# Kernel tuning notes

Hardware: AMD Instinct MI355X
Metric: run time of the kernel (lower is better)

Reference implementation:

```python
import jax, jax.numpy as jnp
import numpy as np

D_MODEL = 1024
N_HEADS = 16
HEAD_DIM = D_MODEL // N_HEADS
MAX_POS = 4096
ROPE_BASE = 10000.0
NEG_INF = -1e30


def _rope_cache(max_pos, head_dim, base):
    inv_freq = 1.0 / (base ** (np.arange(0, head_dim, 2, dtype=np.float32) / head_dim))
    t = np.arange(max_pos, dtype=np.float32)[:, None] * inv_freq[None, :]  # [P, D/2]
    cos = np.repeat(np.cos(t), 2, axis=-1)  # [P, D] (repeat_interleave)
    sin = np.repeat(np.sin(t), 2, axis=-1)
    return jnp.asarray(cos), jnp.asarray(sin)

COS_CACHE, SIN_CACHE = _rope_cache(MAX_POS, HEAD_DIM, ROPE_BASE)


def _rotate_half(x):
    # interleaved pairs: (x0,x1,x2,x3,...) -> (-x1,x0,-x3,x2,...)
    x1 = x[..., ::2]
    x2 = x[..., 1::2]
    return jnp.stack((-x2, x1), axis=-1).reshape(x.shape)


def setup_inputs() -> dict:
    key = jax.random.key(0)
    k0, k1, k2 = jax.random.split(key, 3)
    B, S = 4, 1024
    hidden_states = jax.random.normal(k0, (B, S, D_MODEL), dtype=jnp.float32)
    positions = jnp.arange(S, dtype=jnp.int64 if jax.config.jax_enable_x64 else jnp.int32)
    causal_mask = jnp.triu(jnp.ones((S, S), dtype=bool), k=1)  # True above diagonal -> masked
    # learned params (torch nn.Linear weight layout: [out, in], y = x @ W.T)
    Wqkv = jax.random.normal(k1, (3 * D_MODEL, D_MODEL), dtype=jnp.float32) * (D_MODEL ** -0.5)
    Wout = jax.random.normal(k2, (D_MODEL, D_MODEL), dtype=jnp.float32) * (D_MODEL ** -0.5)
    return {"hidden_states": hidden_states, "positions": positions,
            "causal_mask": causal_mask, "Wqkv": Wqkv, "Wout": Wout}


def reference(hidden_states, positions, causal_mask, Wqkv, Wout):
    B, S, D = hidden_states.shape
    qkv = hidden_states @ Wqkv.T                                   # [B,S,3D]
    qkv = qkv.reshape(B, S, 3, N_HEADS, HEAD_DIM)
    qkv = jnp.transpose(qkv, (2, 0, 3, 1, 4))                      # [3,B,H,S,Dh]
    q, k, v = qkv[0], qkv[1], qkv[2]
    # RoPE
    pos = jnp.clip(positions, 0, MAX_POS - 1)
    if pos.ndim == 1:
        pos = pos[None, :]
    cos = COS_CACHE[pos][:, None, :, :].astype(q.dtype)            # [B,1,S,Dh]
    sin = SIN_CACHE[pos][:, None, :, :].astype(q.dtype)
    q = q * cos + _rotate_half(q) * sin
    k = k * cos + _rotate_half(k) * sin
    # SDPA with causal bias (F.scaled_dot_product_attention default scaling)
    scale = HEAD_DIM ** -0.5
    scores = jnp.einsum('bhqd,bhkd->bhqk', q, k) * scale           # [B,H,S,S]
    scores = jnp.where(causal_mask[None, None, :, :], NEG_INF, scores)
    probs = jax.nn.softmax(scores, axis=-1)
    attn = jnp.einsum('bhqk,bhkd->bhqd', probs, v)                 # [B,H,S,Dh]
    attn = jnp.transpose(attn, (0, 2, 1, 3)).reshape(B, S, D)
    return attn @ Wout.T
```

## Files before the change

kernel.cpp:

```cpp
#include <hip/hip_runtime.h>

typedef __attribute__((ext_vector_type(8))) short short8;
typedef __attribute__((ext_vector_type(4))) float f32x4;

#define MFMA(a, b, c) __builtin_amdgcn_mfma_f32_16x16x32_bf16((a), (b), (c), 0, 0, 0)

#define S_LEN 1024
#define DM 1024
#define NHEADS 16
#define HD 64
#define NBH 64
#define MAXPOS 4096

__device__ __forceinline__ ushort f2bf(float f) {
    unsigned u = __builtin_bit_cast(unsigned, f);
    u += 0x7fffu + ((u >> 16) & 1u);
    return (ushort)(u >> 16);
}
__device__ __forceinline__ float bf2f(ushort h) {
    return __builtin_bit_cast(float, (unsigned)h << 16);
}

__device__ __forceinline__ void gload16(const ushort* g, ushort* l) {
    __builtin_amdgcn_global_load_lds(
        (const __attribute__((address_space(1))) unsigned int*)g,
        (__attribute__((address_space(3))) unsigned int*)l, 16, 0, 0);
}

__global__ __launch_bounds__(256) void k_cvt3(const float4* __restrict__ hs,
                                              const float4* __restrict__ wqkv,
                                              const float4* __restrict__ wout,
                                              ushort4* __restrict__ hsB,
                                              ushort4* __restrict__ wqkvB,
                                              ushort4* __restrict__ woutB,
                                              float* __restrict__ tab) {
    int id = blockIdx.x * 256 + threadIdx.x;
    if (id < 2097152) {
        const float4* src;
        ushort4* dst;
        int off;
        if (id < 1048576)      { src = hs;   dst = hsB;   off = id; }
        else if (id < 1835008) { src = wqkv; dst = wqkvB; off = id - 1048576; }
        else                   { src = wout; dst = woutB; off = id - 1835008; }
        float4 v = src[off];
        ushort4 o;
        o.x = f2bf(v.x); o.y = f2bf(v.y); o.z = f2bf(v.z); o.w = f2bf(v.w);
        dst[off] = o;
    } else {
        int t = id - 2097152;
        int p = t >> 5, i = t & 31;
        float inv = powf(10000.f, -(float)(2 * i) / 64.f);
        float th = (float)p * inv;
        float s, c;
        sincosf(th, &s, &c);
        tab[2 * t] = c;
        tab[2 * t + 1] = s;
    }
}

template <int MODE>
__global__ __launch_bounds__(512, 6) void k_gemm(
    const ushort* __restrict__ A, const ushort* __restrict__ BT,
    float* __restrict__ Cf,
    const int* __restrict__ pos, const float* __restrict__ tab,
    ushort* __restrict__ Qh, ushort* __restrict__ Kh, ushort* __restrict__ Vt,
    int M, int N, int K, int nbx) {
    __shared__ __align__(16) ushort SH[3 * 8192];
    const int tid = threadIdx.x;
    const int lane = tid & 63, wave = tid >> 6;
    const int wr = wave >> 2, wc = wave & 3;
    const int l15 = lane & 15, lhi = lane >> 4;
    const int nby = gridDim.x / nbx;
    const int xcd = blockIdx.x & 7, idx = blockIdx.x >> 3;
    const int Creg = nbx >> 1, Rreg = nby >> 2;
    const int by = (xcd >> 1) * Rreg + idx / Creg;
    const int bx = (xcd & 1) * Creg + idx % Creg;
    const int m0 = by << 7, n0 = bx << 7;

    const int srow = tid >> 2;
    const int scol = (((tid & 3) ^ (srow & 3) ^ ((srow >> 2) & 3)) << 3);
    const int fcol = ((lhi ^ ((l15 & 3) ^ ((l15 >> 2) & 3)))) << 3;

    f32x4 acc[4][2];
#pragma unroll
    for (int i = 0; i < 4; ++i)
#pragma unroll
        for (int j = 0; j < 2; ++j) acc[i][j] = 0;

#define STAGE(bs, kb)                                                           \
    do {                                                                        \
        ushort* bb = SH + (bs) * 8192;                                          \
        gload16(&A[(size_t)(m0 + srow) * K + (kb) + scol], bb + tid * 8);       \
        gload16(&BT[(size_t)(n0 + srow) * K + (kb) + scol],                     \
                bb + 4096 + tid * 8);                                           \
    } while (0)

    const int nk = K >> 5;
    STAGE(0, 0);
    STAGE(1, 32);
    int bi = 0;
    for (int t = 0; t < nk; ++t) {
        if (t + 1 < nk) {
            asm volatile("s_waitcnt vmcnt(2)" ::: "memory");
        } else {
            asm volatile("s_waitcnt vmcnt(0)" ::: "memory");
        }
        __builtin_amdgcn_s_barrier();
        __builtin_amdgcn_sched_barrier(0);
        if (t + 2 < nk) {
            int bs = bi + 2;
            if (bs >= 3) bs -= 3;
            STAGE(bs, (t + 2) << 5);
        }
        const ushort* bufA = SH + bi * 8192;
        const ushort* bufB = bufA + 4096;
        short8 a[4], b[2];
#pragma unroll
        for (int fm = 0; fm < 4; ++fm)
            a[fm] = *(const short8*)&bufA[(wr * 64 + fm * 16 + l15) * 32 + fcol];
#pragma unroll
        for (int fn = 0; fn < 2; ++fn)
            b[fn] = *(const short8*)&bufB[(wc * 32 + fn * 16 + l15) * 32 + fcol];
#pragma unroll
        for (int fm = 0; fm < 4; ++fm)
#pragma unroll
            for (int fn = 0; fn < 2; ++fn)
                acc[fm][fn] = MFMA(a[fm], b[fn], acc[fm][fn]);
        bi = (bi == 2) ? 0 : bi + 1;
    }
#undef STAGE
    __syncthreads();

    if (MODE == 0) {
#pragma unroll
        for (int fm = 0; fm < 4; ++fm)
#pragma unroll
            for (int fn = 0; fn < 2; ++fn)
#pragma unroll
                for (int i = 0; i < 4; ++i) {
                    int row = m0 + wr * 64 + fm * 16 + lhi * 4 + i;
                    int col = n0 + wc * 32 + fn * 16 + l15;
                    Cf[(size_t)row * N + col] = acc[fm][fn][i];
                }
    } else {
        const int sec = n0 >> 10;
        if (sec < 2) {
            ushort* dstb = sec == 0 ? Qh : Kh;
            const float qs = sec == 0 ? 0.125f : 1.0f;
#pragma unroll
            for (int fm = 0; fm < 4; ++fm)
#pragma unroll
                for (int i = 0; i < 4; ++i) {
                    const int row = m0 + wr * 64 + fm * 16 + lhi * 4 + i;
                    const int b = row >> 10, s = row & 1023;
                    int p = pos[s];
                    p = p < 0 ? 0 : (p > MAXPOS - 1 ? MAXPOS - 1 : p);
#pragma unroll
                    for (int fn = 0; fn < 2; ++fn) {
                        const int col = n0 + wc * 32 + fn * 16 + l15;
                        const int cw = col & 1023;
                        const int h = cw >> 6, d = cw & 63;
                        const float c  = tab[((size_t)p * 32 + (d >> 1)) * 2];
                        const float sn = tab[((size_t)p * 32 + (d >> 1)) * 2 + 1];
                        const float v = acc[fm][fn][i];
                        const float pr = __shfl_xor(v, 1);
                        const float o = (d & 1) ? (v * c + pr * sn) : (v * c - pr * sn);
                        dstb[((size_t)((b * 16 + h) * 1024 + s)) * 64 + d] = f2bf(o * qs);
                    }
                }
        } else {
            ushort (*T)[132] = (ushort(*)[132]) & SH[0];
#pragma unroll
            for (int fm = 0; fm < 4; ++fm)
#pragma unroll
                for (int fn = 0; fn < 2; ++fn)
#pragma unroll
                    for (int i = 0; i < 4; ++i)
                        T[wr * 64 + fm * 16 + lhi * 4 + i][wc * 32 + fn * 16 + l15] =
                            f2bf(acc[fm][fn][i]);
            __syncthreads();
            const int b = m0 >> 10, s0 = m0 & 1023;
            const int dd = tid & 127, grp = tid >> 7;
            const int hv = ((n0 & 1023) >> 6) + (dd >> 6);
            const int d = dd & 63;
            ushort* dst = Vt + ((size_t)(b * 16 + hv) * 64 + d) * S_LEN + s0;
#pragma unroll
            for (int j = 0; j < 4; ++j) {
                const int ch = grp * 4 + j;
                __align__(16) ushort tmp[8];
#pragma unroll
                for (int e = 0; e < 8; ++e) tmp[e] = T[ch * 8 + e][dd];
                *(uint4*)&dst[ch * 8] = *(uint4*)tmp;
            }
        }
    }
}

__global__ __launch_bounds__(256, 2) void k_attn(const ushort* __restrict__ Qh,
                                                 const ushort* __restrict__ Kh,
                                                 const ushort* __restrict__ Vt,
                                                 ushort* __restrict__ attnB) {
    __shared__ __align__(16) ushort Ks[2][128][64];
    __shared__ __align__(16) ushort Vs[2][64][128];
    __shared__ __align__(16) ushort P[4][16][128];
    const int bh = blockIdx.x;
    const int g  = blockIdx.y;
    const int gA = g, gB = 15 - g;
    const int nkbA = (gA + 2) >> 1;
    const int nkbB = (gB + 2) >> 1;
    const int tid = threadIdx.x;
    const int wave = tid >> 6, lane = tid & 63;
    const int l15 = lane & 15, lhi = lane >> 4;
    const int b = bh >> 4, h = bh & 15;
    const ushort* Qp = Qh + (size_t)bh * S_LEN * 64;
    const ushort* Kp = Kh + (size_t)bh * S_LEN * 64;
    const ushort* Vp = Vt + (size_t)bh * 64 * S_LEN;
    const int qbA = (gA << 6) + (wave << 4);
    const int qbB = (gB << 6) + (wave << 4);
    const int qrowbA = qbA + lhi * 4;
    const int qrowbB = qbB + lhi * 4;

    ushort* KsF = &Ks[0][0][0];
    ushort* VsF = &Vs[0][0][0];
    ushort* Pw  = &P[wave][0][0];

    short8 aQA0 = *(const short8*)&Qp[(size_t)(qbA + l15) * 64 + lhi * 8];
    short8 aQA1 = *(const short8*)&Qp[(size_t)(qbA + l15) * 64 + 32 + lhi * 8];
    short8 aQB0 = *(const short8*)&Qp[(size_t)(qbB + l15) * 64 + lhi * 8];
    short8 aQB1 = *(const short8*)&Qp[(size_t)(qbB + l15) * 64 + 32 + lhi * 8];

    short8 ones;
#pragma unroll
    for (int j = 0; j < 8; ++j) ones[j] = (short)0x3F80;

    f32x4 OA0{}, OA1{}, OA2{}, OA3{}, ssumA{};
    f32x4 OB0{}, OB1{}, OB2{}, OB3{}, ssumB{};

#define STAGEKV(bo, k0s)                                                        \
    do {                                                                        \
        _Pragma("unroll") for (int k = 0; k < 4; ++k) {                         \
            const int u = tid + k * 256;                                        \
            const int r = u >> 3, c = u & 7;                                    \
            gload16(&Kp[(size_t)((k0s) + r) * 64 + ((c ^ (r & 7)) << 3)],       \
                    KsF + (bo) + u * 8);                                        \
        }                                                                       \
        _Pragma("unroll") for (int k = 0; k < 4; ++k) {                         \
            const int u = tid + k * 256;                                        \
            const int r = u >> 4, c = u & 15;                                   \
            const int cs = c ^ (r & 7);                                         \
            gload16(&Vp[(size_t)r * S_LEN + (k0s) + cs * 8], VsF + (bo) + u * 8); \
        }                                                                       \
    } while (0)

#define LDSK(s, kk) (*(const short8*)(KsF + (cur << 13) + ((((s) << 4) + l15) << 6) + \
                                      (((((kk) << 2) + lhi) ^ (l15 & 7)) << 3)))
#define LDSV(n, kk) (*(const short8*)(VsF + (cur << 13) + ((((n) << 4) + l15) << 7) + \
                                      (((((kk) << 2) + lhi) ^ (l15 & 7)) << 3)))

    STAGEKV(0, 0);
    __syncthreads();

    int cur = 0;
    for (int kb = 0; kb < nkbB; ++kb) {
        const int k0 = kb << 7;
        if (kb + 1 < nkbB) STAGEKV((cur ^ 1) << 13, k0 + 128);

#define TILE_WORK(AQ0, AQ1, QROWB, NKB, O0, O1, O2, O3, SSUM)                   \
    if (kb < (NKB)) {                                                           \
        f32x4 sc[8];                                                            \
        __builtin_amdgcn_s_setprio(1);                                          \
        _Pragma("unroll") for (int s = 0; s < 8; ++s) {                         \
            sc[s] = f32x4{0.f, 0.f, 0.f, 0.f};                                  \
            sc[s] = MFMA(AQ0, LDSK(s, 0), sc[s]);                               \
            sc[s] = MFMA(AQ1, LDSK(s, 1), sc[s]);                               \
        }                                                                       \
        __builtin_amdgcn_s_setprio(0);                                          \
        if (kb == (NKB) - 1) {                                                  \
            _Pragma("unroll") for (int s = 0; s < 8; ++s)                       \
                _Pragma("unroll") for (int i = 0; i < 4; ++i) {                 \
                    float v = sc[s][i];                                         \
                    if (k0 + s * 16 + l15 > (QROWB) + i) v = -1e30f;            \
                    const int row = lhi * 4 + i;                                \
                    Pw[row * 128 +                                              \
                       (((s * 2 + (l15 >> 3)) ^ (row & 7)) << 3) + (l15 & 7)] = \
                        f2bf(__expf(v - 8.f));                                  \
                }                                                               \
        } else {                                                                \
            _Pragma("unroll") for (int s = 0; s < 8; ++s)                       \
                _Pragma("unroll") for (int i = 0; i < 4; ++i) {                 \
                    const int row = lhi * 4 + i;                                \
                    Pw[row * 128 +                                              \
                       (((s * 2 + (l15 >> 3)) ^ (row & 7)) << 3) + (l15 & 7)] = \
                        f2bf(__expf(sc[s][i] - 8.f));                           \
                }                                                               \
        }                                                                       \
        short8 aP[4];                                                           \
        _Pragma("unroll") for (int kk = 0; kk < 4; ++kk)                        \
            aP[kk] = *(const short8*)&Pw[l15 * 128 +                            \
                                         ((((kk << 2) + lhi) ^ (l15 & 7)) << 3)]; \
        __builtin_amdgcn_s_setprio(1);                                          \
        _Pragma("unroll") for (int kk = 0; kk < 4; ++kk) {                      \
            SSUM = MFMA(aP[kk], ones, SSUM);                                    \
            O0 = MFMA(aP[kk], LDSV(0, kk), O0);                                 \
            O1 = MFMA(aP[kk], LDSV(1, kk), O1);                                 \
            O2 = MFMA(aP[kk], LDSV(2, kk), O2);                                 \
            O3 = MFMA(aP[kk], LDSV(3, kk), O3);                                 \
        }                                                                       \
        __builtin_amdgcn_s_setprio(0);                                          \
    }

        TILE_WORK(aQA0, aQA1, qrowbA, nkbA, OA0, OA1, OA2, OA3, ssumA)
        TILE_WORK(aQB0, aQB1, qrowbB, nkbB, OB0, OB1, OB2, OB3, ssumB)
#undef TILE_WORK

        __syncthreads();
        cur ^= 1;
    }
#undef LDSK
#undef LDSV
#undef STAGEKV

#define WOUT(OV, N, QB, INV)                                                   \
    _Pragma("unroll") for (int i = 0; i < 4; ++i) {                            \
        int row = (QB) + lhi * 4 + i;                                          \
        attnB[((size_t)(b * S_LEN + row)) * DM + h * 64 + (N) * 16 + l15] =    \
            f2bf(OV[i] * INV[i]);                                              \
    }
    {
        f32x4 invA, invB;
#pragma unroll
        for (int i = 0; i < 4; ++i) {
            invA[i] = 1.f / ssumA[i];
            invB[i] = 1.f / ssumB[i];
        }
        WOUT(OA0, 0, qbA, invA) WOUT(OA1, 1, qbA, invA)
        WOUT(OA2, 2, qbA, invA) WOUT(OA3, 3, qbA, invA)
        WOUT(OB0, 0, qbB, invB) WOUT(OB1, 1, qbB, invB)
        WOUT(OB2, 2, qbB, invB) WOUT(OB3, 3, qbB, invB)
    }
#undef WOUT
}

extern "C" void kernel_launch(void* const* d_in, const int* in_sizes, int n_in,
                              void* d_out, int out_size, void* d_ws, size_t ws_size,
                              hipStream_t stream) {
    (void)in_sizes; (void)n_in; (void)out_size; (void)ws_size;
    const float* hs   = (const float*)d_in[0];
    const int*   pos  = (const int*)d_in[1];
    const float* Wqkv = (const float*)d_in[3];
    const float* Wout = (const float*)d_in[4];
    float* out = (float*)d_out;

    char* ws = (char*)d_ws;
    size_t off = 0;
    ushort* hsB   = (ushort*)(ws + off); off += (size_t)4096 * 1024 * 2;
    ushort* WqkvB = (ushort*)(ws + off); off += (size_t)3072 * 1024 * 2;
    ushort* WoutB = (ushort*)(ws + off); off += (size_t)1024 * 1024 * 2;
    ushort* Qh    = (ushort*)(ws + off); off += (size_t)NBH * 1024 * 64 * 2;
    ushort* Kh    = (ushort*)(ws + off); off += (size_t)NBH * 1024 * 64 * 2;
    ushort* Vt    = (ushort*)(ws + off); off += (size_t)NBH * 64 * 1024 * 2;
    ushort* attnB = (ushort*)(ws + off); off += (size_t)4096 * 1024 * 2;
    float*  tab   = (float*)(ws + off);  off += (size_t)4096 * 32 * 2 * 4;

    k_cvt3<<<8704, 256, 0, stream>>>((const float4*)hs, (const float4*)Wqkv,
                                     (const float4*)Wout, (ushort4*)hsB,
                                     (ushort4*)WqkvB, (ushort4*)WoutB, tab);

    k_gemm<1><<<768, 512, 0, stream>>>(hsB, WqkvB, nullptr, pos, tab,
                                       Qh, Kh, Vt, 4096, 3072, 1024, 24);

    k_attn<<<dim3(64, 8), 256, 0, stream>>>(Qh, Kh, Vt, attnB);

    k_gemm<0><<<256, 512, 0, stream>>>(attnB, WoutB, out, nullptr, nullptr,
                                       nullptr, nullptr, nullptr, 4096, 1024, 1024, 8);
}
```

Baseline: 90.46 us.

## Switch GEMM to 32x32x16 MFMA with 4-wave blocks and 64x64 warp tiles

The projection GEMMs move from 8 waves each computing 64x32 with 16x16x32 MFMAs to 4 waves each computing 64x64 with 32x32x16 MFMAs. The 128x128 block tile stays, so each thread now issues two global-to-LDS loads per operand per stage, and the LDS swizzle and epilogue index maps are rewritten to match the 32x32 accumulator layout. The aim is more reuse per LDS fragment read and fewer MFMA issues per FLOP, at the cost of more accumulator registers per thread and fewer waves to hide latency.

```diff
diff --git a/kernel.cpp b/kernel.cpp
--- a/kernel.cpp
+++ b/kernel.cpp
@@ -2,8 +2,10 @@
 
 typedef __attribute__((ext_vector_type(8))) short short8;
 typedef __attribute__((ext_vector_type(4))) float f32x4;
+typedef __attribute__((ext_vector_type(16))) float f32x16;
 
 #define MFMA(a, b, c) __builtin_amdgcn_mfma_f32_16x16x32_bf16((a), (b), (c), 0, 0, 0)
+#define MFMA32(a, b, c) __builtin_amdgcn_mfma_f32_32x32x16_bf16((a), (b), (c), 0, 0, 0)
 
 #define S_LEN 1024
 #define DM 1024
@@ -59,7 +61,7 @@
 }
 
 template <int MODE>
-__global__ __launch_bounds__(512, 6) void k_gemm(
+__global__ __launch_bounds__(256, 3) void k_gemm(
     const ushort* __restrict__ A, const ushort* __restrict__ BT,
     float* __restrict__ Cf,
     const int* __restrict__ pos, const float* __restrict__ tab,
@@ -68,8 +70,8 @@
     __shared__ __align__(16) ushort SH[3 * 8192];
     const int tid = threadIdx.x;
     const int lane = tid & 63, wave = tid >> 6;
-    const int wr = wave >> 2, wc = wave & 3;
-    const int l15 = lane & 15, lhi = lane >> 4;
+    const int wr = wave >> 1, wc = wave & 1;
+    const int l31 = lane & 31, lh = lane >> 5;
     const int nby = gridDim.x / nbx;
     const int xcd = blockIdx.x & 7, idx = blockIdx.x >> 3;
     const int Creg = nbx >> 1, Rreg = nby >> 2;
@@ -78,12 +80,12 @@
     const int m0 = by << 7, n0 = bx << 7;
 
     const int srow = tid >> 2;
-    const int scol = (((tid & 3) ^ (srow & 3) ^ ((srow >> 2) & 3)) << 3);
-    const int fcol = ((lhi ^ ((l15 & 3) ^ ((l15 >> 2) & 3)))) << 3;
-
-    f32x4 acc[4][2];
-#pragma unroll
-    for (int i = 0; i < 4; ++i)
+    const int scol = (((tid >> 2) & 3) ^ ((tid >> 4) & 3) ^ (tid & 3)) << 3;
+    const int swz = (lane & 3) ^ ((lane >> 2) & 3);
+
+    f32x16 acc[2][2];
+#pragma unroll
+    for (int i = 0; i < 2; ++i)
 #pragma unroll
         for (int j = 0; j < 2; ++j) acc[i][j] = 0;
 
@@ -91,8 +93,12 @@
     do {                                                                        \
         ushort* bb = SH + (bs) * 8192;                                          \
         gload16(&A[(size_t)(m0 + srow) * K + (kb) + scol], bb + tid * 8);       \
+        gload16(&A[(size_t)(m0 + 64 + srow) * K + (kb) + scol],                 \
+                bb + 2048 + tid * 8);                                           \
         gload16(&BT[(size_t)(n0 + srow) * K + (kb) + scol],                     \
                 bb + 4096 + tid * 8);                                           \
+        gload16(&BT[(size_t)(n0 + 64 + srow) * K + (kb) + scol],                \
+                bb + 6144 + tid * 8);                                           \
     } while (0)
 
     const int nk = K >> 5;
@@ -101,7 +107,7 @@
     int bi = 0;
     for (int t = 0; t < nk; ++t) {
         if (t + 1 < nk) {
-            asm volatile("s_waitcnt vmcnt(2)" ::: "memory");
+            asm volatile("s_waitcnt vmcnt(4)" ::: "memory");
         } else {
             asm volatile("s_waitcnt vmcnt(0)" ::: "memory");
         }
@@ -114,18 +120,26 @@
         }
         const ushort* bufA = SH + bi * 8192;
         const ushort* bufB = bufA + 4096;
-        short8 a[4], b[2];
-#pragma unroll
-        for (int fm = 0; fm < 4; ++fm)
-            a[fm] = *(const short8*)&bufA[(wr * 64 + fm * 16 + l15) * 32 + fcol];
-#pragma unroll
-        for (int fn = 0; fn < 2; ++fn)
-            b[fn] = *(const short8*)&bufB[(wc * 32 + fn * 16 + l15) * 32 + fcol];
-#pragma unroll
-        for (int fm = 0; fm < 4; ++fm)
-#pragma unroll
-            for (int fn = 0; fn < 2; ++fn)
-                acc[fm][fn] = MFMA(a[fm], b[fn], acc[fm][fn]);
+        short8 aF[2][2], bF[2][2];
+#pragma unroll
+        for (int tm = 0; tm < 2; ++tm)
+#pragma unroll
+            for (int ks = 0; ks < 2; ++ks)
+                aF[tm][ks] = *(const short8*)&bufA[(wr * 64 + tm * 32 + l31) * 32 +
+                                                   (((lh + 2 * ks) ^ swz) << 3)];
+#pragma unroll
+        for (int tn = 0; tn < 2; ++tn)
+#pragma unroll
+            for (int ks = 0; ks < 2; ++ks)
+                bF[tn][ks] = *(const short8*)&bufB[(wc * 64 + tn * 32 + l31) * 32 +
+                                                   (((lh + 2 * ks) ^ swz) << 3)];
+#pragma unroll
+        for (int tm = 0; tm < 2; ++tm)
+#pragma unroll
+            for (int tn = 0; tn < 2; ++tn)
+#pragma unroll
+                for (int ks = 0; ks < 2; ++ks)
+                    acc[tm][tn] = MFMA32(aF[tm][ks], bF[tn][ks], acc[tm][tn]);
         bi = (bi == 2) ? 0 : bi + 1;
     }
 #undef STAGE
@@ -133,14 +147,14 @@
 
     if (MODE == 0) {
 #pragma unroll
-        for (int fm = 0; fm < 4; ++fm)
-#pragma unroll
-            for (int fn = 0; fn < 2; ++fn)
-#pragma unroll
-                for (int i = 0; i < 4; ++i) {
-                    int row = m0 + wr * 64 + fm * 16 + lhi * 4 + i;
-                    int col = n0 + wc * 32 + fn * 16 + l15;
-                    Cf[(size_t)row * N + col] = acc[fm][fn][i];
+        for (int tm = 0; tm < 2; ++tm)
+#pragma unroll
+            for (int tn = 0; tn < 2; ++tn)
+#pragma unroll
+                for (int reg = 0; reg < 16; ++reg) {
+                    int row = m0 + wr * 64 + tm * 32 + (reg & 3) + 8 * (reg >> 2) + 4 * lh;
+                    int col = n0 + wc * 64 + tn * 32 + l31;
+                    Cf[(size_t)row * N + col] = acc[tm][tn][reg];
                 }
     } else {
         const int sec = n0 >> 10;
@@ -148,21 +162,21 @@
             ushort* dstb = sec == 0 ? Qh : Kh;
             const float qs = sec == 0 ? 0.125f : 1.0f;
 #pragma unroll
-            for (int fm = 0; fm < 4; ++fm)
-#pragma unroll
-                for (int i = 0; i < 4; ++i) {
-                    const int row = m0 + wr * 64 + fm * 16 + lhi * 4 + i;
+            for (int tm = 0; tm < 2; ++tm)
+#pragma unroll
+                for (int reg = 0; reg < 16; ++reg) {
+                    const int row = m0 + wr * 64 + tm * 32 + (reg & 3) + 8 * (reg >> 2) + 4 * lh;
                     const int b = row >> 10, s = row & 1023;
                     int p = pos[s];
                     p = p < 0 ? 0 : (p > MAXPOS - 1 ? MAXPOS - 1 : p);
 #pragma unroll
-                    for (int fn = 0; fn < 2; ++fn) {
-                        const int col = n0 + wc * 32 + fn * 16 + l15;
+                    for (int tn = 0; tn < 2; ++tn) {
+                        const int col = n0 + wc * 64 + tn * 32 + l31;
                         const int cw = col & 1023;
                         const int h = cw >> 6, d = cw & 63;
                         const float c  = tab[((size_t)p * 32 + (d >> 1)) * 2];
                         const float sn = tab[((size_t)p * 32 + (d >> 1)) * 2 + 1];
-                        const float v = acc[fm][fn][i];
+                        const float v = acc[tm][tn][reg];
                         const float pr = __shfl_xor(v, 1);
                         const float o = (d & 1) ? (v * c + pr * sn) : (v * c - pr * sn);
                         dstb[((size_t)((b * 16 + h) * 1024 + s)) * 64 + d] = f2bf(o * qs);
@@ -171,22 +185,22 @@
         } else {
             ushort (*T)[132] = (ushort(*)[132]) & SH[0];
 #pragma unroll
-            for (int fm = 0; fm < 4; ++fm)
-#pragma unroll
-                for (int fn = 0; fn < 2; ++fn)
-#pragma unroll
-                    for (int i = 0; i < 4; ++i)
-                        T[wr * 64 + fm * 16 + lhi * 4 + i][wc * 32 + fn * 16 + l15] =
-                            f2bf(acc[fm][fn][i]);
+            for (int tm = 0; tm < 2; ++tm)
+#pragma unroll
+                for (int tn = 0; tn < 2; ++tn)
+#pragma unroll
+                    for (int reg = 0; reg < 16; ++reg)
+                        T[wr * 64 + tm * 32 + (reg & 3) + 8 * (reg >> 2) + 4 * lh]
+                         [wc * 64 + tn * 32 + l31] = f2bf(acc[tm][tn][reg]);
             __syncthreads();
             const int b = m0 >> 10, s0 = m0 & 1023;
-            const int dd = tid & 127, grp = tid >> 7;
+            const int dd = tid & 127, scg = tid >> 7;
             const int hv = ((n0 & 1023) >> 6) + (dd >> 6);
             const int d = dd & 63;
             ushort* dst = Vt + ((size_t)(b * 16 + hv) * 64 + d) * S_LEN + s0;
 #pragma unroll
-            for (int j = 0; j < 4; ++j) {
-                const int ch = grp * 4 + j;
+            for (int j = 0; j < 8; ++j) {
+                const int ch = scg * 8 + j;
                 __align__(16) ushort tmp[8];
 #pragma unroll
                 for (int e = 0; e < 8; ++e) tmp[e] = T[ch * 8 + e][dd];
@@ -366,11 +380,11 @@
                                      (const float4*)Wout, (ushort4*)hsB,
                                      (ushort4*)WqkvB, (ushort4*)WoutB, tab);
 
-    k_gemm<1><<<768, 512, 0, stream>>>(hsB, WqkvB, nullptr, pos, tab,
+    k_gemm<1><<<768, 256, 0, stream>>>(hsB, WqkvB, nullptr, pos, tab,
                                        Qh, Kh, Vt, 4096, 3072, 1024, 24);
 
     k_attn<<<dim3(64, 8), 256, 0, stream>>>(Qh, Kh, Vt, attnB);
 
-    k_gemm<0><<<256, 512, 0, stream>>>(attnB, WoutB, out, nullptr, nullptr,
+    k_gemm<0><<<256, 256, 0, stream>>>(attnB, WoutB, out, nullptr, nullptr,
                                        nullptr, nullptr, nullptr, 4096, 1024, 1024, 8);
 }
```

After: 92.62 us. 2.4% more time.

## Add dedicated output-projection GEMM with smaller tiles and triple-buffered LDS

Applied to the files above, without the earlier changes.

Replaces the shared k_gemm<0> launch for the output projection with a new kernel that uses 128x64 tiles, 256 threads and a 3-stage global_load_lds pipeline with swizzled LDS layout. The launch grows from 256 to 512 blocks, which is meant to fill more of the GPU's CUs for the 4096x1024x1024 GEMM. It also maps blocks to XCDs in rectangular regions for L2 locality. The trade-off is more total global traffic from smaller tiles and a per-tile barrier at each K-step of 32.

```diff
diff --git a/kernel.cpp b/kernel.cpp
--- a/kernel.cpp
+++ b/kernel.cpp
@@ -196,6 +196,91 @@
     }
 }
 
+__global__ __launch_bounds__(256, 4) void k_gemm_out(
+    const ushort* __restrict__ A, const ushort* __restrict__ BT,
+    float* __restrict__ Cf, int M, int N, int K, int nbx) {
+    __shared__ __align__(16) ushort SH[3 * 6144];
+    const int tid = threadIdx.x;
+    const int lane = tid & 63, wave = tid >> 6;
+    const int wr = wave >> 1, wc = wave & 1;
+    const int l15 = lane & 15, lhi = lane >> 4;
+    const int nby = gridDim.x / nbx;
+    const int xcd = blockIdx.x & 7, idx = blockIdx.x >> 3;
+    const int Creg = nbx >> 1, Rreg = nby >> 2;
+    const int by = (xcd >> 1) * Rreg + idx / Creg;
+    const int bx = (xcd & 1) * Creg + idx % Creg;
+    const int m0 = by << 7, n0 = bx << 6;
+
+    const int brow = tid >> 2;
+    const int bcol = (((tid & 3) ^ (brow & 3) ^ ((brow >> 2) & 3)) << 3);
+    const int fcol = ((lhi ^ ((l15 & 3) ^ ((l15 >> 2) & 3)))) << 3;
+
+    f32x4 acc[4][2];
+#pragma unroll
+    for (int i = 0; i < 4; ++i)
+#pragma unroll
+        for (int j = 0; j < 2; ++j) acc[i][j] = 0;
+
+#define STAGE(bs, kb)                                                           \
+    do {                                                                        \
+        ushort* bb = SH + (bs) * 6144;                                          \
+        _Pragma("unroll") for (int k = 0; k < 2; ++k) {                         \
+            const int u = tid + k * 256;                                        \
+            const int r = u >> 2;                                               \
+            const int sc = (((u & 3) ^ (r & 3) ^ ((r >> 2) & 3)) << 3);         \
+            gload16(&A[(size_t)(m0 + r) * K + (kb) + sc], bb + u * 8);          \
+        }                                                                       \
+        gload16(&BT[(size_t)(n0 + brow) * K + (kb) + bcol],                     \
+                bb + 4096 + tid * 8);                                           \
+    } while (0)
+
+    const int nk = K >> 5;
+    STAGE(0, 0);
+    STAGE(1, 32);
+    int bi = 0;
+    for (int t = 0; t < nk; ++t) {
+        if (t + 1 < nk) {
+            asm volatile("s_waitcnt vmcnt(3)" ::: "memory");
+        } else {
+            asm volatile("s_waitcnt vmcnt(0)" ::: "memory");
+        }
+        __builtin_amdgcn_s_barrier();
+        __builtin_amdgcn_sched_barrier(0);
+        if (t + 2 < nk) {
+            int bs = bi + 2;
+            if (bs >= 3) bs -= 3;
+            STAGE(bs, (t + 2) << 5);
+        }
+        const ushort* bufA = SH + bi * 6144;
+        const ushort* bufB = bufA + 4096;
+        short8 a[4], b[2];
+#pragma unroll
+        for (int fm = 0; fm < 4; ++fm)
+            a[fm] = *(const short8*)&bufA[(wr * 64 + fm * 16 + l15) * 32 + fcol];
+#pragma unroll
+        for (int fn = 0; fn < 2; ++fn)
+            b[fn] = *(const short8*)&bufB[(wc * 32 + fn * 16 + l15) * 32 + fcol];
+#pragma unroll
+        for (int fm = 0; fm < 4; ++fm)
+#pragma unroll
+            for (int fn = 0; fn < 2; ++fn)
+                acc[fm][fn] = MFMA(a[fm], b[fn], acc[fm][fn]);
+        bi = (bi == 2) ? 0 : bi + 1;
+    }
+#undef STAGE
+
+#pragma unroll
+    for (int fm = 0; fm < 4; ++fm)
+#pragma unroll
+        for (int fn = 0; fn < 2; ++fn)
+#pragma unroll
+            for (int i = 0; i < 4; ++i) {
+                int row = m0 + wr * 64 + fm * 16 + lhi * 4 + i;
+                int col = n0 + wc * 32 + fn * 16 + l15;
+                Cf[(size_t)row * N + col] = acc[fm][fn][i];
+            }
+}
+
 __global__ __launch_bounds__(256, 2) void k_attn(const ushort* __restrict__ Qh,
                                                  const ushort* __restrict__ Kh,
                                                  const ushort* __restrict__ Vt,
@@ -371,6 +456,5 @@
 
     k_attn<<<dim3(64, 8), 256, 0, stream>>>(Qh, Kh, Vt, attnB);
 
-    k_gemm<0><<<256, 512, 0, stream>>>(attnB, WoutB, out, nullptr, nullptr,
-                                       nullptr, nullptr, nullptr, 4096, 1024, 1024, 8);
-}
+    k_gemm_out<<<512, 256, 0, stream>>>(attnB, WoutB, out, 4096, 1024, 1024, 16);
+}
```

After: 90.89 us. About the same (+0.5%).
